# Kernel optimization log

Hardware: AMD Instinct MI355X
Metric: run time of the kernel (lower is better)

Reference implementation:

```python
import jax, jax.numpy as jnp
import numpy as np

N_NODES = 100000
Z_DIM = 64
N_EDGES = 1000000
H = 64

def setup_inputs() -> dict:
    key = jax.random.key(0)
    k1, k2, k3, k4 = jax.random.split(key, 4)
    z = jax.random.normal(k1, (N_NODES, Z_DIM), dtype=jnp.float32)
    edge = jax.random.randint(k2, (2, N_EDGES), 0, N_NODES, dtype=jnp.int64)
    # Linear params (stored as [in, out] for x @ W + b)
    W1 = jax.random.normal(k3, (2 * Z_DIM, H), dtype=jnp.float32) * (1.0 / np.sqrt(2 * Z_DIM))
    b1 = jnp.zeros((H,), dtype=jnp.float32)
    W2 = jax.random.normal(k4, (H, 1), dtype=jnp.float32) * (1.0 / np.sqrt(H))
    b2 = jnp.zeros((1,), dtype=jnp.float32)
    return {"z": z, "edge": edge, "W1": W1, "b1": b1, "W2": W2, "b2": b2}

def reference(z, edge, W1, b1, W2, b2):
    zi = z[edge[0]]                      # [E, z_dim] gather
    zj = z[edge[1]]                      # [E, z_dim] gather
    h = jnp.concatenate([zi, zj], axis=-1)  # [E, 2*z_dim]
    h = jax.nn.relu(h @ W1 + b1)         # [E, H]
    out = h @ W2 + b2                    # [E, 1]
    return out.squeeze(-1)               # [E]
```

## Files before the change

### kernel.cpp

```cpp
#include <hip/hip_runtime.h>
#include <hip/hip_bf16.h>

typedef unsigned short u16;
typedef unsigned int u32;
typedef __attribute__((ext_vector_type(8))) short bf16x8;
typedef __attribute__((ext_vector_type(8))) float f32x8;
typedef __attribute__((ext_vector_type(2))) unsigned int u32x2;
typedef _Float16 h16x2 __attribute__((ext_vector_type(2)));

static __device__ __forceinline__ u16 f2bf(float f) {
    __hip_bfloat16 b = __float2bfloat16(f);
    return *(u16*)&b;
}
static __device__ __forceinline__ u16 f2h(float f) {
    _Float16 h = (_Float16)f;
    return __builtin_bit_cast(u16, h);
}

static __device__ __forceinline__ void gload_lds16(const void* g, void* l) {
    __builtin_amdgcn_global_load_lds(
        (const __attribute__((address_space(1))) unsigned int*)g,
        (__attribute__((address_space(3))) unsigned int*)l,
        16, 0, 0);
}


__global__ __launch_bounds__(256) void build_wfrag(
    const float* __restrict__ W1, const float* __restrict__ W2,
    u16* __restrict__ wtab)
{
    const int flat = blockIdx.x * 256 + threadIdx.x;
    if (flat < 8192) {
        const int j    = flat & 7;
        const int lane = (flat >> 3) & 63;
        const int ks   = (flat >> 9) & 3;
        const int ct   = flat >> 11;
        const int k = ks * 16 + (lane >> 5) * 8 + j;
        const int c = ct * 32 + (lane & 31);
        const float v = (c < 64) ? W1[(size_t)k * 64 + c]
                                 : W1[(size_t)(64 + k) * 64 + (c - 64)];
        wtab[flat] = f2bf(v);
    } else if (flat < 8256) {
        wtab[flat] = f2h(W2[flat - 8192]);
    }
}

__global__ __launch_bounds__(256, 4) void node_mfma(
    const float* __restrict__ z, const u16* __restrict__ wtab,
    const float* __restrict__ b1, u16* __restrict__ pq, int nNodes)
{
    const int lane   = threadIdx.x & 63;
    const int wave   = threadIdx.x >> 6;
    const int l31    = lane & 31;
    const int half   = lane >> 5;
    const int nodeBase = (blockIdx.x * 4 + wave) * 32;
    if (nodeBase >= nNodes) return;

    __shared__ u16 tile[4][4096];
    char* tb = (char*)&tile[wave][0];

    const char* zbase = (const char*)(z + (size_t)nodeBase * 64);
#pragma unroll
    for (int s = 0; s < 8; ++s) {
        const int r  = 4 * s + (lane >> 4);
        const int bb = (lane & 15) * 16;
        const char* gsrc = zbase + (size_t)r * 256 + (bb ^ ((r & 7) << 4));
        gload_lds16(gsrc, tb + s * 1024);
    }
    asm volatile("s_waitcnt vmcnt(0)" ::: "memory");

    bf16x8 Zf[4];
    const int sw = (l31 & 7) << 4;
#pragma unroll
    for (int ks = 0; ks < 4; ++ks) {
        const int col0 = ks * 64 + half * 32;
        const float4 v0 = *(const float4*)(tb + l31 * 256 + ((col0 +  0) ^ sw));
        const float4 v1 = *(const float4*)(tb + l31 * 256 + ((col0 + 16) ^ sw));
        Zf[ks][0] = (short)f2bf(v0.x); Zf[ks][1] = (short)f2bf(v0.y);
        Zf[ks][2] = (short)f2bf(v0.z); Zf[ks][3] = (short)f2bf(v0.w);
        Zf[ks][4] = (short)f2bf(v1.x); Zf[ks][5] = (short)f2bf(v1.y);
        Zf[ks][6] = (short)f2bf(v1.z); Zf[ks][7] = (short)f2bf(v1.w);
    }

    const bf16x8* wt = (const bf16x8*)wtab;

    for (int pass = 0; pass < 2; ++pass) {
        const int ct0 = 2 * pass;

        bf16x8 Wf[2][4];
#pragma unroll
        for (int c2 = 0; c2 < 2; ++c2)
#pragma unroll
            for (int ks = 0; ks < 4; ++ks)
                Wf[c2][ks] = wt[((ct0 + c2) * 4 + ks) * 64 + lane];

        f32x8 acc[2][2];
#pragma unroll
        for (int c2 = 0; c2 < 2; ++c2) {
            const int ct = ct0 + c2;
            if (ct < 2) {
#pragma unroll
                for (int g = 0; g < 4; ++g) {
                    const float4 bv =
                        *(const float4*)(b1 + ct * 32 + g * 8 + half * 4);
                    acc[c2][g >> 1][4 * (g & 1) + 0] = bv.x;
                    acc[c2][g >> 1][4 * (g & 1) + 1] = bv.y;
                    acc[c2][g >> 1][4 * (g & 1) + 2] = bv.z;
                    acc[c2][g >> 1][4 * (g & 1) + 3] = bv.w;
                }
            } else {
                acc[c2][0] = (f32x8)(0.0f);
                acc[c2][1] = (f32x8)(0.0f);
            }
        }

#pragma unroll
        for (int c2 = 0; c2 < 2; ++c2) {
            typedef __attribute__((ext_vector_type(16))) float f32x16;
            f32x16 a;
#pragma unroll
            for (int r = 0; r < 8; ++r) { a[r] = acc[c2][0][r]; a[8 + r] = acc[c2][1][r]; }
#pragma unroll
            for (int ks = 0; ks < 4; ++ks)
                a = __builtin_amdgcn_mfma_f32_32x32x16_bf16(
                    Wf[c2][ks], Zf[ks], a, 0, 0, 0);
#pragma unroll
            for (int r = 0; r < 8; ++r) { acc[c2][0][r] = a[r]; acc[c2][1][r] = a[8 + r]; }
        }

#pragma unroll
        for (int c2 = 0; c2 < 2; ++c2)
#pragma unroll
            for (int g = 0; g < 4; ++g) {
                const float f0 = acc[c2][g >> 1][4 * (g & 1) + 0];
                const float f1 = acc[c2][g >> 1][4 * (g & 1) + 1];
                const float f2 = acc[c2][g >> 1][4 * (g & 1) + 2];
                const float f3 = acc[c2][g >> 1][4 * (g & 1) + 3];
                const u32 lo = (u32)f2h(f0) | ((u32)f2h(f1) << 16);
                const u32 hi = (u32)f2h(f2) | ((u32)f2h(f3) << 16);
                const int roff = ((ct0 + c2) * 64 + g * 16 + half * 8)
                                 ^ ((l31 & 7) << 4);
                *(u32x2*)(tb + l31 * 256 + roff) = (u32x2){lo, hi};
            }
    }

#pragma unroll
    for (int it = 0; it < 8; ++it) {
        const int c16  = lane + 64 * it;
        const int nd   = c16 >> 4;
        const int roff = ((c16 & 15) * 16) ^ ((nd & 7) << 4);
        const uint4 v = *(const uint4*)(tb + nd * 256 + roff);
        if (nodeBase + nd < nNodes)
            *(uint4*)(pq + (size_t)nodeBase * 128 + (size_t)c16 * 8) = v;
    }
}

__global__ __launch_bounds__(256) void edge_mlp(
    const int* __restrict__ e0, const int* __restrict__ e1,
    const u16* __restrict__ pq, const u16* __restrict__ w2tab,
    const float* __restrict__ b2, float* __restrict__ out, int E)
{
    const int gid = blockIdx.x * 256 + threadIdx.x;
    const int e   = gid >> 2;
    const int sub = gid & 3;
    if (e >= E) return;

    const int i = e0[e];
    const int j = e1[e];

    const uint4* pr = (const uint4*)(pq + (size_t)i * 128);
    const uint4* qr = (const uint4*)(pq + (size_t)j * 128 + 64);
    const uint4 p0 = pr[2 * sub];
    const uint4 p1 = pr[2 * sub + 1];
    const uint4 q0 = qr[2 * sub];
    const uint4 q1 = qr[2 * sub + 1];

    const uint4* wr = (const uint4*)w2tab;
    const uint4 w0 = wr[2 * sub];
    const uint4 w1 = wr[2 * sub + 1];

    const u32 pw[8] = {p0.x, p0.y, p0.z, p0.w, p1.x, p1.y, p1.z, p1.w};
    const u32 qw[8] = {q0.x, q0.y, q0.z, q0.w, q1.x, q1.y, q1.z, q1.w};
    const u32 ww[8] = {w0.x, w0.y, w0.z, w0.w, w1.x, w1.y, w1.z, w1.w};
    const h16x2 hzero = (h16x2){(_Float16)0.0f, (_Float16)0.0f};

    float sum = 0.0f;
#pragma unroll
    for (int c = 0; c < 8; ++c) {
        h16x2 pp = __builtin_bit_cast(h16x2, pw[c]);
        h16x2 qq = __builtin_bit_cast(h16x2, qw[c]);
        h16x2 wc = __builtin_bit_cast(h16x2, ww[c]);
        h16x2 a  = __builtin_elementwise_max(pp + qq, hzero);
#if __has_builtin(__builtin_amdgcn_fdot2)
        sum = __builtin_amdgcn_fdot2(a, wc, sum, false);
#else
        sum = fmaf((float)a[0], (float)wc[0],
              fmaf((float)a[1], (float)wc[1], sum));
#endif
    }

    sum += __shfl_xor(sum, 1);
    sum += __shfl_xor(sum, 2);

    if (sub == 0) out[e] = sum + b2[0];
}

extern "C" void kernel_launch(void* const* d_in, const int* in_sizes, int n_in,
                              void* d_out, int out_size, void* d_ws, size_t ws_size,
                              hipStream_t stream) {
    const float* z  = (const float*)d_in[0];
    const int*   eg = (const int*)d_in[1];
    const float* W1 = (const float*)d_in[2];
    const float* b1 = (const float*)d_in[3];
    const float* W2 = (const float*)d_in[4];
    const float* b2 = (const float*)d_in[5];
    float* out = (float*)d_out;

    const int nNodes = in_sizes[0] / 64;
    const int E      = in_sizes[1] / 2;

    u16* wtab = (u16*)d_ws;
    u16* pq   = (u16*)d_ws + 16384;

    build_wfrag<<<dim3(33), dim3(256), 0, stream>>>(W1, W2, wtab);

    dim3 gA((nNodes + 127) / 128);
    node_mfma<<<gA, dim3(256), 0, stream>>>(z, wtab, b1, pq, nNodes);

    long long tB = (long long)E * 4;
    dim3 gB((unsigned)((tB + 255) / 256));
    edge_mlp<<<gB, dim3(256), 0, stream>>>(eg, eg + E, pq, wtab + 8192, b2, out, E);
}
```

Measured before the change: 120.8 us.

## Partition edges by source-node range to improve cache locality of gathers

Adds a histogram, scan and scatter pass that buckets edges into 8 ranges by source node index and packs (i, j, edge index) into 64-bit records. The edge MLP kernel then assigns blocks per bucket, so each group of blocks gathers from a smaller slice of the node table and that slice can stay cache-resident. The q-row reads and record reads use nontemporal loads. This costs three extra kernel launches plus a full read of the edge list and a write and read of 8 MB of records, and output writes become scattered.

```diff
diff --git a/kernel.cpp b/kernel.cpp
--- a/kernel.cpp
+++ b/kernel.cpp
@@ -3,9 +3,11 @@
 
 typedef unsigned short u16;
 typedef unsigned int u32;
+typedef unsigned long long u64;
 typedef __attribute__((ext_vector_type(8))) short bf16x8;
 typedef __attribute__((ext_vector_type(8))) float f32x8;
 typedef __attribute__((ext_vector_type(2))) unsigned int u32x2;
+typedef __attribute__((ext_vector_type(4))) unsigned int u32x4;
 typedef _Float16 h16x2 __attribute__((ext_vector_type(2)));
 
 static __device__ __forceinline__ u16 f2bf(float f) {
@@ -24,6 +26,8 @@
         16, 0, 0);
 }
 
+
+#define PART_BLOCKS 256
 
 __global__ __launch_bounds__(256) void build_wfrag(
     const float* __restrict__ W1, const float* __restrict__ W2,
@@ -155,54 +159,125 @@
     }
 }
 
-__global__ __launch_bounds__(256) void edge_mlp(
+__global__ __launch_bounds__(256) void edge_histo(
+    const int* __restrict__ e0, u32* __restrict__ cnt, int E, u32 bdiv)
+{
+    __shared__ u32 h[8];
+    if (threadIdx.x < 8) h[threadIdx.x] = 0;
+    __syncthreads();
+    const int chunk = (E + PART_BLOCKS - 1) / PART_BLOCKS;
+    const int start = blockIdx.x * chunk;
+    const int end   = min(E, start + chunk);
+    for (int idx = start + threadIdx.x; idx < end; idx += 256)
+        atomicAdd(&h[(u32)e0[idx] / bdiv], 1u);
+    __syncthreads();
+    if (threadIdx.x < 8) cnt[blockIdx.x * 8 + threadIdx.x] = h[threadIdx.x];
+}
+
+__global__ __launch_bounds__(256) void edge_scan(
+    const u32* __restrict__ cnt, u32* __restrict__ base,
+    u32* __restrict__ bucketBase, u32* __restrict__ bucketCnt)
+{
+    __shared__ u32 arr[256];
+    const int t = threadIdx.x;
+    u32 acc = 0;
+    for (int b = 0; b < 8; ++b) {
+        const u32 v = cnt[t * 8 + b];
+        arr[t] = v; __syncthreads();
+        for (int ofs = 1; ofs < 256; ofs <<= 1) {
+            const u32 x = (t >= ofs) ? arr[t - ofs] : 0;
+            __syncthreads();
+            arr[t] += x; __syncthreads();
+        }
+        const u32 incl  = arr[t];
+        const u32 total = arr[255];
+        base[t * 8 + b] = acc + incl - v;
+        if (t == 0) { bucketBase[b] = acc; bucketCnt[b] = total; }
+        acc += total;
+        __syncthreads();
+    }
+}
+
+__global__ __launch_bounds__(256) void edge_scatter(
     const int* __restrict__ e0, const int* __restrict__ e1,
-    const u16* __restrict__ pq, const u16* __restrict__ w2tab,
-    const float* __restrict__ b2, float* __restrict__ out, int E)
-{
-    const int gid = blockIdx.x * 256 + threadIdx.x;
-    const int e   = gid >> 2;
-    const int sub = gid & 3;
-    if (e >= E) return;
-
-    const int i = e0[e];
-    const int j = e1[e];
-
-    const uint4* pr = (const uint4*)(pq + (size_t)i * 128);
-    const uint4* qr = (const uint4*)(pq + (size_t)j * 128 + 64);
-    const uint4 p0 = pr[2 * sub];
-    const uint4 p1 = pr[2 * sub + 1];
-    const uint4 q0 = qr[2 * sub];
-    const uint4 q1 = qr[2 * sub + 1];
+    const u32* __restrict__ base, u64* __restrict__ rec, int E, u32 bdiv)
+{
+    __shared__ u32 cur[8];
+    if (threadIdx.x < 8) cur[threadIdx.x] = base[blockIdx.x * 8 + threadIdx.x];
+    __syncthreads();
+    const int chunk = (E + PART_BLOCKS - 1) / PART_BLOCKS;
+    const int start = blockIdx.x * chunk;
+    const int end   = min(E, start + chunk);
+    for (int idx = start + threadIdx.x; idx < end; idx += 256) {
+        const u32 i = (u32)e0[idx];
+        const u32 j = (u32)e1[idx];
+        const u32 pos = atomicAdd(&cur[i / bdiv], 1u);
+        rec[pos] = (u64)i | ((u64)j << 17) | ((u64)idx << 34);
+    }
+}
+
+__global__ __launch_bounds__(256) void edge_mlp_part(
+    const u64* __restrict__ rec, const u32* __restrict__ bucketBase,
+    const u32* __restrict__ bucketCnt, const u16* __restrict__ pq,
+    const u16* __restrict__ w2tab, const float* __restrict__ b2,
+    float* __restrict__ out)
+{
+    const u32 b  = blockIdx.x & 7;
+    const u32 s  = blockIdx.x >> 3;
+    const u32 rb = bucketBase[b];
+    const u32 rc = bucketCnt[b];
+    const int tid  = threadIdx.x;
+    const u32 egrp = (u32)(tid >> 2);
+    const int sub  = tid & 3;
 
     const uint4* wr = (const uint4*)w2tab;
     const uint4 w0 = wr[2 * sub];
     const uint4 w1 = wr[2 * sub + 1];
-
-    const u32 pw[8] = {p0.x, p0.y, p0.z, p0.w, p1.x, p1.y, p1.z, p1.w};
-    const u32 qw[8] = {q0.x, q0.y, q0.z, q0.w, q1.x, q1.y, q1.z, q1.w};
-    const u32 ww[8] = {w0.x, w0.y, w0.z, w0.w, w1.x, w1.y, w1.z, w1.w};
+    const float bias = b2[0];
     const h16x2 hzero = (h16x2){(_Float16)0.0f, (_Float16)0.0f};
 
-    float sum = 0.0f;
-#pragma unroll
-    for (int c = 0; c < 8; ++c) {
-        h16x2 pp = __builtin_bit_cast(h16x2, pw[c]);
-        h16x2 qq = __builtin_bit_cast(h16x2, qw[c]);
-        h16x2 wc = __builtin_bit_cast(h16x2, ww[c]);
-        h16x2 a  = __builtin_elementwise_max(pp + qq, hzero);
+    for (u32 o = s * 64u; o < rc; o += 64u * 256u) {
+        const u32 ei = o + egrp;
+        if (ei < rc) {
+            const u64 r = __builtin_nontemporal_load(
+                (const u64*)&rec[rb + ei]);
+            const u32 i = (u32)r & 131071u;
+            const u32 j = ((u32)(r >> 17)) & 131071u;
+            const u32 e = (u32)(r >> 34);
+
+            const uint4* pr = (const uint4*)(pq + (size_t)i * 128);
+            const u32x4* qr = (const u32x4*)(pq + (size_t)j * 128 + 64);
+            const uint4 p0 = pr[2 * sub];
+            const uint4 p1 = pr[2 * sub + 1];
+            const u32x4 q0 = __builtin_nontemporal_load(qr + 2 * sub);
+            const u32x4 q1 = __builtin_nontemporal_load(qr + 2 * sub + 1);
+
+            const u32 pw[8] = {p0.x, p0.y, p0.z, p0.w, p1.x, p1.y, p1.z, p1.w};
+            const u32 qw[8] = {q0[0], q0[1], q0[2], q0[3],
+                               q1[0], q1[1], q1[2], q1[3]};
+            const u32 ww[8] = {w0.x, w0.y, w0.z, w0.w, w1.x, w1.y, w1.z, w1.w};
+
+            float sum = 0.0f;
+#pragma unroll
+            for (int c = 0; c < 8; ++c) {
+                h16x2 pp = __builtin_bit_cast(h16x2, pw[c]);
+                h16x2 qq = __builtin_bit_cast(h16x2, qw[c]);
+                h16x2 wc = __builtin_bit_cast(h16x2, ww[c]);
+                h16x2 a  = __builtin_elementwise_max(pp + qq, hzero);
 #if __has_builtin(__builtin_amdgcn_fdot2)
-        sum = __builtin_amdgcn_fdot2(a, wc, sum, false);
+                sum = __builtin_amdgcn_fdot2(a, wc, sum, false);
 #else
-        sum = fmaf((float)a[0], (float)wc[0],
-              fmaf((float)a[1], (float)wc[1], sum));
+                sum = fmaf((float)a[0], (float)wc[0],
+                      fmaf((float)a[1], (float)wc[1], sum));
 #endif
-    }
-
-    sum += __shfl_xor(sum, 1);
-    sum += __shfl_xor(sum, 2);
-
-    if (sub == 0) out[e] = sum + b2[0];
+            }
+
+            sum += __shfl_xor(sum, 1);
+            sum += __shfl_xor(sum, 2);
+
+            if (sub == 0) out[e] = sum + bias;
+        }
+    }
 }
 
 extern "C" void kernel_launch(void* const* d_in, const int* in_sizes, int n_in,
@@ -219,15 +294,27 @@
     const int nNodes = in_sizes[0] / 64;
     const int E      = in_sizes[1] / 2;
 
+    char* wsb = (char*)d_ws;
     u16* wtab = (u16*)d_ws;
     u16* pq   = (u16*)d_ws + 16384;
+    u64* rec  = (u64*)(wsb + 32768 + (size_t)nNodes * 256);
+    u32* cnt  = (u32*)((char*)rec + (size_t)E * 8);
+    u32* base = cnt + PART_BLOCKS * 8;
+    u32* bucketBase = base + PART_BLOCKS * 8;
+    u32* bucketCnt  = bucketBase + 8;
+
+    const u32 bdiv = (u32)((nNodes + 7) / 8);
 
     build_wfrag<<<dim3(33), dim3(256), 0, stream>>>(W1, W2, wtab);
 
     dim3 gA((nNodes + 127) / 128);
     node_mfma<<<gA, dim3(256), 0, stream>>>(z, wtab, b1, pq, nNodes);
 
-    long long tB = (long long)E * 4;
-    dim3 gB((unsigned)((tB + 255) / 256));
-    edge_mlp<<<gB, dim3(256), 0, stream>>>(eg, eg + E, pq, wtab + 8192, b2, out, E);
-}
+    edge_histo<<<dim3(PART_BLOCKS), dim3(256), 0, stream>>>(eg, cnt, E, bdiv);
+    edge_scan<<<dim3(1), dim3(256), 0, stream>>>(cnt, base, bucketBase, bucketCnt);
+    edge_scatter<<<dim3(PART_BLOCKS), dim3(256), 0, stream>>>(
+        eg, eg + E, base, rec, E, bdiv);
+
+    edge_mlp_part<<<dim3(2048), dim3(256), 0, stream>>>(
+        rec, bucketBase, bucketCnt, pq, wtab + 8192, b2, out);
+}
```

After: 162.3 us. +34.3%, slower.
